# Performance work log

Measured on AMD Instinct MI355X. Metric: run time of the kernel, lower is better.

The kernel has to match this reference:

```python
import jax, jax.numpy as jnp
import numpy as np

N = 50000      # n_nodes
E = 300000     # n_edges
R = 32         # n_relations
D = 256        # embedding_dim
H = 128        # bilstm_hidden_size (2H == D so gate dims line up, as the source requires)
I = 64         # input_dim (time-series feature dim)
B = 4096       # batch
S = 50         # seq_len
HOPS = 2       # context_hops


def setup_inputs() -> dict:
    key = jax.random.key(0)
    ks = jax.random.split(key, 20)
    sc = 0.02
    inp = {
        "ts": jax.random.normal(ks[0], (B, S, I), jnp.float32),
        "node_emb": jax.random.normal(ks[1], (N, D), jnp.float32) * sc,
        "rel_w": jax.random.normal(ks[2], (R, D), jnp.float32) * sc + 1.0,
        "gate_W": jax.random.normal(ks[3], (D, 2 * D), jnp.float32) * sc,
        "gate_b": jnp.zeros((D,), jnp.float32),
        "risk_W1": jax.random.normal(ks[4], (D, D), jnp.float32) * sc,
        "risk_b1": jnp.zeros((D,), jnp.float32),
        "risk_W2": jax.random.normal(ks[5], (D, D), jnp.float32) * sc,
        "risk_b2": jnp.zeros((D,), jnp.float32),
        # BiLSTM encoder params (torch gate order i,f,g,o), fwd + bwd directions
        "Wih_f": jax.random.normal(ks[6], (4 * H, I), jnp.float32) * sc,
        "Whh_f": jax.random.normal(ks[7], (4 * H, H), jnp.float32) * sc,
        "b_f": jnp.zeros((4 * H,), jnp.float32),
        "Wih_b": jax.random.normal(ks[8], (4 * H, I), jnp.float32) * sc,
        "Whh_b": jax.random.normal(ks[9], (4 * H, H), jnp.float32) * sc,
        "b_b": jnp.zeros((4 * H,), jnp.float32),
        "edge_index": jax.random.randint(ks[10], (2, E), 0, N, jnp.int32),
        "edge_type": jax.random.randint(ks[11], (E,), 0, R, jnp.int32),
        "node_indexes": jax.random.randint(ks[12], (B,), 0, N, jnp.int32),
    }
    return inp


def _lstm_dir(x, Wih, Whh, b, reverse):
    # x: [B, S, I] -> outputs [B, S, H]
    def step(carry, xt):
        h, c = carry
        g = xt @ Wih.T + h @ Whh.T + b          # [B, 4H]
        i, f, gg, o = jnp.split(g, 4, axis=-1)
        c = jax.nn.sigmoid(f) * c + jax.nn.sigmoid(i) * jnp.tanh(gg)
        h = jax.nn.sigmoid(o) * jnp.tanh(c)
        return (h, c), h
    h0 = jnp.zeros((x.shape[0], Whh.shape[1]), x.dtype)
    xs = jnp.swapaxes(x, 0, 1)                   # [S, B, I]
    _, hs = jax.lax.scan(step, (h0, h0), xs, reverse=reverse)
    return jnp.swapaxes(hs, 0, 1)                # [B, S, H]


def _gcn(emb, head, tail, edge_type, rel_w, n_hops):
    # relation-weighted multi-hop message passing: gather -> relation scale -> scatter-mean
    deg = jax.ops.segment_sum(jnp.ones((head.shape[0],), emb.dtype), head, num_segments=N)
    deg = jnp.clip(deg, 1.0)[:, None]
    out = emb
    acc = emb
    for _ in range(n_hops):
        msg = out[tail] * rel_w[edge_type]                      # [E, D]
        out = jax.ops.segment_sum(msg, head, num_segments=N) / deg
        acc = acc + out
    return acc / (n_hops + 1.0)


def reference(ts, node_emb, rel_w, gate_W, gate_b, risk_W1, risk_b1, risk_W2,
              risk_b2, Wih_f, Whh_f, b_f, Wih_b, Whh_b, b_b,
              edge_index, edge_type, node_indexes):
    head, tail = edge_index[0], edge_index[1]
    all_emb = _gcn(node_emb, head, tail, edge_type, rel_w, HOPS)
    struct = all_emb[node_indexes]                              # [B, D]
    # BiLSTM encoder, temporal embedding = mean over time of [B,S,2H]
    hf = _lstm_dir(ts, Wih_f, Whh_f, b_f, reverse=False)
    hb = _lstm_dir(ts, Wih_b, Whh_b, b_b, reverse=True)
    temporal = jnp.concatenate([hf, hb], axis=-1).mean(axis=1)  # [B, 2H] == [B, D]
    cat = jnp.concatenate([struct, temporal], axis=-1)          # [B, 2D]
    gate = jax.nn.sigmoid(cat @ gate_W.T + gate_b)              # [B, D]
    merged = gate * struct + (1.0 - gate) * temporal
    risk = jnp.tanh(merged @ risk_W1.T + risk_b1) @ risk_W2.T + risk_b2
    return jax.nn.sigmoid(risk.sum(axis=-1))                    # [B]
```

## Files before the change

### kernel.cpp

```cpp
#include <hip/hip_runtime.h>

#define N_NODES 50000
#define N_EDGES 300000
#define DIM 256
#define HID 128
#define INP 64
#define BATCH 4096
#define SEQ 50
#define SCAN_BLOCKS 196

typedef float f32x2 __attribute__((ext_vector_type(2)));
typedef float f32x4 __attribute__((ext_vector_type(4)));
typedef __bf16 bf16x2 __attribute__((ext_vector_type(2)));
typedef __bf16 bf16x8 __attribute__((ext_vector_type(8)));

__device__ __forceinline__ float sigmoidf_(float x) {
    return __builtin_amdgcn_rcpf(1.0f + __expf(-x));
}
__device__ __forceinline__ float tanhf_(float x) {
    return 1.0f - 2.0f * __builtin_amdgcn_rcpf(1.0f + __expf(2.0f * x));
}


__global__ void k_hist(const int* __restrict__ head, int* __restrict__ deg) {
    int e = blockIdx.x * 256 + threadIdx.x;
    if (e < N_EDGES) atomicAdd(&deg[head[e]], 1);
}

__global__ void k_bsum(const int* __restrict__ deg, int* __restrict__ bsum) {
    __shared__ int red[256];
    int n = blockIdx.x * 256 + threadIdx.x;
    red[threadIdx.x] = (n < N_NODES) ? deg[n] : 0;
    __syncthreads();
    for (int st = 128; st > 0; st >>= 1) {
        if (threadIdx.x < st) red[threadIdx.x] += red[threadIdx.x + st];
        __syncthreads();
    }
    if (threadIdx.x == 0) bsum[blockIdx.x] = red[0];
}

__global__ void k_scanb(const int* __restrict__ bsum, int* __restrict__ boff) {
    __shared__ int s[256];
    int i = threadIdx.x;
    int v = (i < SCAN_BLOCKS) ? bsum[i] : 0;
    s[i] = v;
    __syncthreads();
    for (int st = 1; st < 256; st <<= 1) {
        int add = (i >= st) ? s[i - st] : 0;
        __syncthreads();
        s[i] += add;
        __syncthreads();
    }
    boff[i] = s[i] - v;
}

__global__ void k_scan2(const int* __restrict__ deg, const int* __restrict__ boff,
                        int* __restrict__ offsets, int* __restrict__ cursor) {
    __shared__ int s[256];
    int i = threadIdx.x;
    int n = blockIdx.x * 256 + i;
    int v = (n < N_NODES) ? deg[n] : 0;
    s[i] = v;
    __syncthreads();
    for (int st = 1; st < 256; st <<= 1) {
        int add = (i >= st) ? s[i - st] : 0;
        __syncthreads();
        s[i] += add;
        __syncthreads();
    }
    if (n < N_NODES) {
        int off = boff[blockIdx.x] + s[i] - v;
        offsets[n] = off;
        cursor[n] = off;
    }
    if (n == 0) offsets[N_NODES] = N_EDGES;
}

__global__ void k_place(const int* __restrict__ head, const int* __restrict__ tail,
                        const int* __restrict__ etype, int* __restrict__ cursor,
                        int* __restrict__ sorted) {
    int e = blockIdx.x * 256 + threadIdx.x;
    if (e >= N_EDGES) return;
    int h = head[e];
    int pos = atomicAdd(&cursor[h], 1);
    sorted[pos] = tail[e] | (etype[e] << 16);
}

__global__ void k_flag(const int* __restrict__ nidx, const int* __restrict__ offsets,
                       const int* __restrict__ sorted, char* __restrict__ flag) {
    int b = blockIdx.x * 256 + threadIdx.x;
    if (b >= BATCH) return;
    int n = nidx[b];
    flag[n] = 1;
    int s = offsets[n], e = offsets[n + 1];
    for (int j = s; j < e; j++) flag[sorted[j] & 0xFFFF] = 1;
}

__global__ void k_gather(const int* __restrict__ offsets, const int* __restrict__ sorted,
                         const float* __restrict__ relw, const float* __restrict__ src,
                         const char* __restrict__ flag, float* __restrict__ dst) {
    int tid = threadIdx.x;
    int w = tid >> 6, lane = tid & 63;
    int n = blockIdx.x * 4 + w;
    if (n >= N_NODES) return;
    if (!flag[n]) return;
    int s = offsets[n], e = offsets[n + 1];
    f32x4 acc0 = (f32x4){0.f, 0.f, 0.f, 0.f};
    f32x4 acc1 = (f32x4){0.f, 0.f, 0.f, 0.f};
    f32x4 acc2 = (f32x4){0.f, 0.f, 0.f, 0.f};
    f32x4 acc3 = (f32x4){0.f, 0.f, 0.f, 0.f};
    int j = s;
    for (; j + 4 <= e; j += 4) {
        int p0 = sorted[j], p1 = sorted[j + 1], p2 = sorted[j + 2], p3 = sorted[j + 3];
        f32x4 v0 = *(const f32x4*)(src + (size_t)(p0 & 0xFFFF) * DIM + lane * 4);
        f32x4 v1 = *(const f32x4*)(src + (size_t)(p1 & 0xFFFF) * DIM + lane * 4);
        f32x4 v2 = *(const f32x4*)(src + (size_t)(p2 & 0xFFFF) * DIM + lane * 4);
        f32x4 v3 = *(const f32x4*)(src + (size_t)(p3 & 0xFFFF) * DIM + lane * 4);
        acc0 += v0 * *(const f32x4*)(relw + (p0 >> 16) * DIM + lane * 4);
        acc1 += v1 * *(const f32x4*)(relw + (p1 >> 16) * DIM + lane * 4);
        acc2 += v2 * *(const f32x4*)(relw + (p2 >> 16) * DIM + lane * 4);
        acc3 += v3 * *(const f32x4*)(relw + (p3 >> 16) * DIM + lane * 4);
    }
    for (; j < e; j++) {
        int p0 = sorted[j];
        f32x4 v0 = *(const f32x4*)(src + (size_t)(p0 & 0xFFFF) * DIM + lane * 4);
        acc0 += v0 * *(const f32x4*)(relw + (p0 >> 16) * DIM + lane * 4);
    }
    acc0 = (acc0 + acc1) + (acc2 + acc3);
    float inv = 1.0f / fmaxf((float)(e - s), 1.0f);
    *(f32x4*)(dst + (size_t)n * DIM + lane * 4) = acc0 * inv;
}

__global__ void k_gather2(const int* __restrict__ nidx, const int* __restrict__ offsets,
                          const int* __restrict__ sorted, const float* __restrict__ relw,
                          const float* __restrict__ out1, const float* __restrict__ emb,
                          float* __restrict__ structb) {
    int tid = threadIdx.x;
    int w = tid >> 6, lane = tid & 63;
    int b = blockIdx.x * 4 + w;
    int n = nidx[b];
    int s = offsets[n], e = offsets[n + 1];
    f32x4 acc0 = (f32x4){0.f, 0.f, 0.f, 0.f};
    f32x4 acc1 = (f32x4){0.f, 0.f, 0.f, 0.f};
    f32x4 acc2 = (f32x4){0.f, 0.f, 0.f, 0.f};
    f32x4 acc3 = (f32x4){0.f, 0.f, 0.f, 0.f};
    int j = s;
    for (; j + 4 <= e; j += 4) {
        int p0 = sorted[j], p1 = sorted[j + 1], p2 = sorted[j + 2], p3 = sorted[j + 3];
        f32x4 v0 = *(const f32x4*)(out1 + (size_t)(p0 & 0xFFFF) * DIM + lane * 4);
        f32x4 v1 = *(const f32x4*)(out1 + (size_t)(p1 & 0xFFFF) * DIM + lane * 4);
        f32x4 v2 = *(const f32x4*)(out1 + (size_t)(p2 & 0xFFFF) * DIM + lane * 4);
        f32x4 v3 = *(const f32x4*)(out1 + (size_t)(p3 & 0xFFFF) * DIM + lane * 4);
        acc0 += v0 * *(const f32x4*)(relw + (p0 >> 16) * DIM + lane * 4);
        acc1 += v1 * *(const f32x4*)(relw + (p1 >> 16) * DIM + lane * 4);
        acc2 += v2 * *(const f32x4*)(relw + (p2 >> 16) * DIM + lane * 4);
        acc3 += v3 * *(const f32x4*)(relw + (p3 >> 16) * DIM + lane * 4);
    }
    for (; j < e; j++) {
        int p0 = sorted[j];
        f32x4 v0 = *(const f32x4*)(out1 + (size_t)(p0 & 0xFFFF) * DIM + lane * 4);
        acc0 += v0 * *(const f32x4*)(relw + (p0 >> 16) * DIM + lane * 4);
    }
    acc0 = (acc0 + acc1) + (acc2 + acc3);
    float inv = 1.0f / fmaxf((float)(e - s), 1.0f);
    f32x4 o2 = acc0 * inv;
    f32x4 e0 = *(const f32x4*)(emb + (size_t)n * DIM + lane * 4);
    f32x4 o1 = *(const f32x4*)(out1 + (size_t)n * DIM + lane * 4);
    *(f32x4*)(structb + (size_t)b * DIM + lane * 4) = (e0 + o1 + o2) * (1.0f / 3.0f);
}

__global__ void k_w2frag(const float* __restrict__ Wih_f, const float* __restrict__ Whh_f,
                         const float* __restrict__ Wih_b, const float* __restrict__ Whh_b,
                         __bf16* __restrict__ w2) {
    int idx = blockIdx.x * 256 + threadIdx.x;
    int dir = idx / 98304;
    int rem = idx % 98304;
    int frag = rem >> 9;
    int within = rem & 511;
    int lane = within >> 3, j = within & 7;
    int kc = frag % 6;
    int wg = frag / 6;
    int g = wg & 3, w = wg >> 2;
    int n = g * 128 + w * 16 + (lane & 15);
    int k = kc * 32 + (lane >> 4) * 8 + j;
    const float* Wih = dir ? Wih_b : Wih_f;
    const float* Whh = dir ? Whh_b : Whh_f;
    float v = (k < 64) ? Wih[n * 64 + k] : Whh[n * 128 + (k - 64)];
    w2[idx] = (__bf16)v;
}

__global__ void k_packw(const float* __restrict__ W, __bf16* __restrict__ dst,
                        int K, int total) {
    int idx = blockIdx.x * 256 + threadIdx.x;
    if (idx >= total) return;
    int frag = idx >> 9, within = idx & 511;
    int lane = within >> 3, j = within & 7;
    int kcN = K >> 5;
    int kc = frag % kcN, T = frag / kcN;
    int n = T * 16 + (lane & 15);
    int k = kc * 32 + (lane >> 4) * 8 + j;
    dst[idx] = (__bf16)W[(size_t)n * K + k];
}

__launch_bounds__(512)
__global__ void k_lstm(const float* __restrict__ ts, const __bf16* __restrict__ w2frag,
                       const float* __restrict__ b_f, const float* __restrict__ b_b,
                       float* __restrict__ temporal) {
    int dir = blockIdx.y;
    int btile = blockIdx.x;
    int tid = threadIdx.x;
    int w = tid >> 6;
    int lane = tid & 63;
    int col = lane & 15, quad = lane >> 4;

    __shared__ __align__(16) __bf16 A[16][200];

    for (int i = tid; i < 16 * 128; i += 512) {
        A[i >> 7][64 + (i & 127)] = (__bf16)0.0f;
    }

    const float* bias = dir ? b_b : b_f;
    float bv[4];
#pragma unroll
    for (int g = 0; g < 4; g++) {
        bv[g] = bias[g * 128 + w * 16 + col];
    }

    const __bf16* wbase = w2frag + (size_t)dir * 98304 + (size_t)w * 12288;
    bf16x8 wreg[24];
#pragma unroll
    for (int f = 0; f < 24; f++) {
        wreg[f] = *(const bf16x8*)(wbase + (f << 9) + lane * 8);
    }

    int sm = tid >> 5, sc = (tid & 31) * 2;
    const float* xbase = ts + ((size_t)(btile * 16 + sm) * SEQ) * INP + sc;
    f32x2 xpre = *(const f32x2*)(xbase + (size_t)(dir ? (SEQ - 1) : 0) * INP);

    f32x4 c_reg = (f32x4){0.f, 0.f, 0.f, 0.f};
    f32x4 hsum  = (f32x4){0.f, 0.f, 0.f, 0.f};
    int hoff = 64 + w * 16 + col;
    __syncthreads();

    for (int t = 0; t < SEQ; t++) {
        {
            bf16x2 xv;
            xv[0] = (__bf16)xpre.x; xv[1] = (__bf16)xpre.y;
            *(bf16x2*)&A[sm][sc] = xv;
        }
        if (t + 1 < SEQ) {
            int tt = dir ? (SEQ - 2 - t) : (t + 1);
            xpre = *(const f32x2*)(xbase + (size_t)tt * INP);
        }
        __syncthreads();

        f32x4 acc[4];
#pragma unroll
        for (int g = 0; g < 4; g++) {
            acc[g] = (f32x4){bv[g], bv[g], bv[g], bv[g]};
        }
#pragma unroll
        for (int kc = 0; kc < 6; kc++) {
            bf16x8 a0 = *(const bf16x8*)&A[col][kc * 32 + quad * 8];
#pragma unroll
            for (int g = 0; g < 4; g++) {
                acc[g] = __builtin_amdgcn_mfma_f32_16x16x32_bf16(a0, wreg[g * 6 + kc], acc[g], 0, 0, 0);
            }
        }
        __syncthreads();

#pragma unroll
        for (int r = 0; r < 4; r++) {
            float iv = acc[0][r];
            float fv = acc[1][r];
            float gv = acc[2][r];
            float ov = acc[3][r];
            float c = sigmoidf_(fv) * c_reg[r] + sigmoidf_(iv) * tanhf_(gv);
            float h = sigmoidf_(ov) * tanhf_(c);
            c_reg[r] = c;
            hsum[r] += h;
            A[quad * 4 + r][hoff] = (__bf16)h;
        }
    }

#pragma unroll
    for (int r = 0; r < 4; r++) {
        int b = btile * 16 + quad * 4 + r;
        int j = w * 16 + col;
        temporal[(size_t)b * 256 + dir * 128 + j] = hsum[r] * (1.0f / SEQ);
    }
}


__global__ void k_w2sum(const float* __restrict__ W2, const float* __restrict__ b2,
                        float* __restrict__ w2s) {
    int k = threadIdx.x;
    int bb = blockIdx.x;
    float s = 0.0f;
#pragma unroll
    for (int n = 0; n < 32; n++) s += W2[(size_t)(bb * 32 + n) * 256 + k];
    atomicAdd(&w2s[k], s);
    if (bb == 0) {
        __shared__ float red[256];
        red[k] = b2[k];
        __syncthreads();
        for (int st = 128; st > 0; st >>= 1) {
            if (k < st) red[k] += red[k + st];
            __syncthreads();
        }
        if (k == 0) atomicAdd(&w2s[256], red[0]);
    }
}

__launch_bounds__(256)
__global__ void k_head(const float* __restrict__ structb, const float* __restrict__ temporal,
                       const __bf16* __restrict__ gwp, const __bf16* __restrict__ w1p,
                       const float* __restrict__ gate_b, const float* __restrict__ risk_b1,
                       const float* __restrict__ w2s, float* __restrict__ out) {
    int bt = blockIdx.x;
    int tid = threadIdx.x;
    int w = tid >> 6, lane = tid & 63;
    int col = lane & 15, quad = lane >> 4;

    __shared__ __align__(16) __bf16 cat[16][520];
    __shared__ __align__(16) __bf16 mbuf[16][264];
    __shared__ float sacc[16];

    for (int i = tid; i < 16 * 512; i += 256) {
        int m = i >> 9, k = i & 511;
        int b = bt * 16 + m;
        float v = (k < 256) ? structb[(size_t)b * 256 + k]
                            : temporal[(size_t)b * 256 + (k - 256)];
        cat[m][k] = (__bf16)v;
    }
    if (tid < 16) sacc[tid] = 0.0f;
    __syncthreads();

    f32x4 acc[4];
#pragma unroll
    for (int ct = 0; ct < 4; ct++) {
        float b = gate_b[w * 64 + ct * 16 + col];
        acc[ct] = (f32x4){b, b, b, b};
    }
#pragma unroll
    for (int kc = 0; kc < 16; kc++) {
        bf16x8 a = *(const bf16x8*)&cat[col][kc * 32 + quad * 8];
#pragma unroll
        for (int ct = 0; ct < 4; ct++) {
            bf16x8 bf = *(const bf16x8*)(gwp + (((w * 4 + ct) * 16 + kc) << 9) + lane * 8);
            acc[ct] = __builtin_amdgcn_mfma_f32_16x16x32_bf16(a, bf, acc[ct], 0, 0, 0);
        }
    }
#pragma unroll
    for (int ct = 0; ct < 4; ct++) {
        int n = w * 64 + ct * 16 + col;
#pragma unroll
        for (int r = 0; r < 4; r++) {
            int m = quad * 4 + r;
            int b = bt * 16 + m;
            float g = sigmoidf_(acc[ct][r]);
            float s = structb[(size_t)b * 256 + n];
            float tm = temporal[(size_t)b * 256 + n];
            mbuf[m][n] = (__bf16)(g * s + (1.0f - g) * tm);
        }
    }
    __syncthreads();

    f32x4 acc2[4];
#pragma unroll
    for (int ct = 0; ct < 4; ct++) {
        float b = risk_b1[w * 64 + ct * 16 + col];
        acc2[ct] = (f32x4){b, b, b, b};
    }
#pragma unroll
    for (int kc = 0; kc < 8; kc++) {
        bf16x8 a = *(const bf16x8*)&mbuf[col][kc * 32 + quad * 8];
#pragma unroll
        for (int ct = 0; ct < 4; ct++) {
            bf16x8 bf = *(const bf16x8*)(w1p + (((w * 4 + ct) * 8 + kc) << 9) + lane * 8);
            acc2[ct] = __builtin_amdgcn_mfma_f32_16x16x32_bf16(a, bf, acc2[ct], 0, 0, 0);
        }
    }
    float part[4] = {0.f, 0.f, 0.f, 0.f};
#pragma unroll
    for (int ct = 0; ct < 4; ct++) {
        int n = w * 64 + ct * 16 + col;
        float wv = w2s[n];
#pragma unroll
        for (int r = 0; r < 4; r++) {
            part[r] += tanhf_(acc2[ct][r]) * wv;
        }
    }
#pragma unroll
    for (int off = 1; off < 16; off <<= 1) {
#pragma unroll
        for (int r = 0; r < 4; r++) part[r] += __shfl_xor(part[r], off, 64);
    }
    if (col == 0) {
#pragma unroll
        for (int r = 0; r < 4; r++) atomicAdd(&sacc[quad * 4 + r], part[r]);
    }
    __syncthreads();
    if (tid < 16) out[bt * 16 + tid] = sigmoidf_(sacc[tid] + w2s[256]);
}


extern "C" void kernel_launch(void* const* d_in, const int* in_sizes, int n_in,
                              void* d_out, int out_size, void* d_ws, size_t ws_size,
                              hipStream_t stream) {
    const float* ts       = (const float*)d_in[0];
    const float* node_emb = (const float*)d_in[1];
    const float* rel_w    = (const float*)d_in[2];
    const float* gate_W   = (const float*)d_in[3];
    const float* gate_b   = (const float*)d_in[4];
    const float* risk_W1  = (const float*)d_in[5];
    const float* risk_b1  = (const float*)d_in[6];
    const float* risk_W2  = (const float*)d_in[7];
    const float* risk_b2  = (const float*)d_in[8];
    const float* Wih_f    = (const float*)d_in[9];
    const float* Whh_f    = (const float*)d_in[10];
    const float* b_f      = (const float*)d_in[11];
    const float* Wih_b    = (const float*)d_in[12];
    const float* Whh_b    = (const float*)d_in[13];
    const float* b_b      = (const float*)d_in[14];
    const int* edge_index = (const int*)d_in[15];
    const int* edge_type  = (const int*)d_in[16];
    const int* node_idx   = (const int*)d_in[17];
    const int* head = edge_index;
    const int* tail = edge_index + N_EDGES;
    float* out = (float*)d_out;

    char* ws = (char*)d_ws;
    const size_t o_deg      = 0;
    const size_t o_flagbuf  = 200704;
    const size_t o_bsum     = o_flagbuf + 50176;
    const size_t o_boff     = o_bsum + 1024;
    const size_t o_offsets  = o_boff + 1024;
    const size_t o_cursor   = o_offsets + 200960;
    const size_t o_sorted   = o_cursor + 200704;
    const size_t o_out1     = o_sorted + 1200128;
    const size_t o_temporal = o_out1 + 51200000;
    const size_t o_struct   = o_temporal + 4194304;
    const size_t o_gwp      = o_struct + 4194304;
    const size_t o_w1p      = o_gwp + 262144;
    const size_t o_w2s      = o_w1p + 131072;
    const size_t o_w2frag   = o_w2s + 2048;

    int*    deg      = (int*)(ws + o_deg);
    char*   flag     = (char*)(ws + o_flagbuf);
    int*    bsum     = (int*)(ws + o_bsum);
    int*    boff     = (int*)(ws + o_boff);
    int*    offsets  = (int*)(ws + o_offsets);
    int*    cursor   = (int*)(ws + o_cursor);
    int*    sorted   = (int*)(ws + o_sorted);
    float*  out1     = (float*)(ws + o_out1);
    float*  temporal = (float*)(ws + o_temporal);
    float*  structb  = (float*)(ws + o_struct);
    __bf16* gwp      = (__bf16*)(ws + o_gwp);
    __bf16* w1p      = (__bf16*)(ws + o_w1p);
    float*  w2s      = (float*)(ws + o_w2s);
    __bf16* w2frag   = (__bf16*)(ws + o_w2frag);

    hipMemsetAsync(ws, 0, o_flagbuf + 50176, stream);
    hipMemsetAsync(w2s, 0, 2048, stream);

    k_w2frag<<<768, 256, 0, stream>>>(Wih_f, Whh_f, Wih_b, Whh_b, w2frag);
    k_packw<<<512, 256, 0, stream>>>(gate_W, gwp, 512, 256 * 512);
    k_packw<<<256, 256, 0, stream>>>(risk_W1, w1p, 256, 256 * 256);
    k_w2sum<<<8, 256, 0, stream>>>(risk_W2, risk_b2, w2s);
    k_hist<<<(N_EDGES + 255) / 256, 256, 0, stream>>>(head, deg);
    k_bsum<<<SCAN_BLOCKS, 256, 0, stream>>>(deg, bsum);
    k_scanb<<<1, 256, 0, stream>>>(bsum, boff);
    k_scan2<<<SCAN_BLOCKS, 256, 0, stream>>>(deg, boff, offsets, cursor);
    k_place<<<(N_EDGES + 255) / 256, 256, 0, stream>>>(head, tail, edge_type, cursor, sorted);
    k_flag<<<BATCH / 256, 256, 0, stream>>>(node_idx, offsets, sorted, flag);
    k_gather<<<(N_NODES + 3) / 4, 256, 0, stream>>>(offsets, sorted, rel_w, node_emb, flag, out1);
    k_lstm<<<dim3(BATCH / 16, 2), 512, 0, stream>>>(ts, w2frag, b_f, b_b, temporal);
    k_gather2<<<BATCH / 4, 256, 0, stream>>>(node_idx, offsets, sorted, rel_w, out1, node_emb, structb);
    k_head<<<BATCH / 16, 256, 0, stream>>>(structb, temporal, gwp, w1p, gate_b, risk_b1, w2s, out);
}
```

Baseline: 353.9 us.

## Interleave two batch tiles per LSTM block and fuse prep kernels into one launch

The LSTM kernel now handles two independent 16-row batch tiles per block and interleaves them. Each tile's MFMA matmul overlaps with the other tile's gate nonlinearities, using double-buffered shared memory, so the serial recurrence latency is hidden. This halves the grid to 128x2 blocks, which may underfill the GPU's compute units. Separately, the weight packing, W2 row-sum and buffer zeroing are merged into a single prep kernel, replacing two memsets and four launches.

```diff
diff --git a/kernel.cpp b/kernel.cpp
--- a/kernel.cpp
+++ b/kernel.cpp
@@ -19,6 +19,68 @@
 }
 __device__ __forceinline__ float tanhf_(float x) {
     return 1.0f - 2.0f * __builtin_amdgcn_rcpf(1.0f + __expf(2.0f * x));
+}
+
+__global__ void k_prep(const float* __restrict__ Wih_f, const float* __restrict__ Whh_f,
+                       const float* __restrict__ Wih_b, const float* __restrict__ Whh_b,
+                       const float* __restrict__ gate_W, const float* __restrict__ risk_W1,
+                       const float* __restrict__ risk_W2, const float* __restrict__ risk_b2,
+                       __bf16* __restrict__ w2frag, __bf16* __restrict__ gwp,
+                       __bf16* __restrict__ w1p, float* __restrict__ w2s,
+                       int* __restrict__ deg, int* __restrict__ flagi) {
+    __shared__ float red[256];
+    int bid = blockIdx.x, tid = threadIdx.x;
+    if (bid < 768) {
+        int idx = bid * 256 + tid;
+        int dir = idx / 98304;
+        int rem = idx % 98304;
+        int frag = rem >> 9;
+        int within = rem & 511;
+        int lane = within >> 3, j = within & 7;
+        int kc = frag % 6;
+        int wg = frag / 6;
+        int g = wg & 3, w = wg >> 2;
+        int n = g * 128 + w * 16 + (lane & 15);
+        int k = kc * 32 + (lane >> 4) * 8 + j;
+        const float* Wih = dir ? Wih_b : Wih_f;
+        const float* Whh = dir ? Whh_b : Whh_f;
+        float v = (k < 64) ? Wih[n * 64 + k] : Whh[n * 128 + (k - 64)];
+        w2frag[idx] = (__bf16)v;
+    } else if (bid < 1280) {
+        int idx = (bid - 768) * 256 + tid;
+        int frag = idx >> 9, within = idx & 511;
+        int lane = within >> 3, j = within & 7;
+        int kc = frag % 16, T = frag / 16;
+        int n = T * 16 + (lane & 15);
+        int k = kc * 32 + (lane >> 4) * 8 + j;
+        gwp[idx] = (__bf16)gate_W[(size_t)n * 512 + k];
+    } else if (bid < 1536) {
+        int idx = (bid - 1280) * 256 + tid;
+        int frag = idx >> 9, within = idx & 511;
+        int lane = within >> 3, j = within & 7;
+        int kc = frag % 8, T = frag / 8;
+        int n = T * 16 + (lane & 15);
+        int k = kc * 32 + (lane >> 4) * 8 + j;
+        w1p[idx] = (__bf16)risk_W1[(size_t)n * 256 + k];
+    } else if (bid == 1536) {
+        int k = tid;
+        float s = 0.0f;
+        for (int n = 0; n < 256; n++) s += risk_W2[(size_t)n * 256 + k];
+        w2s[k] = s;
+        red[k] = risk_b2[k];
+        __syncthreads();
+        for (int st = 128; st > 0; st >>= 1) {
+            if (k < st) red[k] += red[k + st];
+            __syncthreads();
+        }
+        if (k == 0) w2s[256] = red[0];
+    } else if (bid < 1733) {
+        int i = (bid - 1537) * 256 + tid;
+        if (i < N_NODES) deg[i] = 0;
+    } else {
+        int i = (bid - 1733) * 256 + tid;
+        flagi[i] = 0;
+    }
 }
 
 
@@ -169,39 +231,6 @@
     *(f32x4*)(structb + (size_t)b * DIM + lane * 4) = (e0 + o1 + o2) * (1.0f / 3.0f);
 }
 
-__global__ void k_w2frag(const float* __restrict__ Wih_f, const float* __restrict__ Whh_f,
-                         const float* __restrict__ Wih_b, const float* __restrict__ Whh_b,
-                         __bf16* __restrict__ w2) {
-    int idx = blockIdx.x * 256 + threadIdx.x;
-    int dir = idx / 98304;
-    int rem = idx % 98304;
-    int frag = rem >> 9;
-    int within = rem & 511;
-    int lane = within >> 3, j = within & 7;
-    int kc = frag % 6;
-    int wg = frag / 6;
-    int g = wg & 3, w = wg >> 2;
-    int n = g * 128 + w * 16 + (lane & 15);
-    int k = kc * 32 + (lane >> 4) * 8 + j;
-    const float* Wih = dir ? Wih_b : Wih_f;
-    const float* Whh = dir ? Whh_b : Whh_f;
-    float v = (k < 64) ? Wih[n * 64 + k] : Whh[n * 128 + (k - 64)];
-    w2[idx] = (__bf16)v;
-}
-
-__global__ void k_packw(const float* __restrict__ W, __bf16* __restrict__ dst,
-                        int K, int total) {
-    int idx = blockIdx.x * 256 + threadIdx.x;
-    if (idx >= total) return;
-    int frag = idx >> 9, within = idx & 511;
-    int lane = within >> 3, j = within & 7;
-    int kcN = K >> 5;
-    int kc = frag % kcN, T = frag / kcN;
-    int n = T * 16 + (lane & 15);
-    int k = kc * 32 + (lane >> 4) * 8 + j;
-    dst[idx] = (__bf16)W[(size_t)n * K + k];
-}
-
 __launch_bounds__(512)
 __global__ void k_lstm(const float* __restrict__ ts, const __bf16* __restrict__ w2frag,
                        const float* __restrict__ b_f, const float* __restrict__ b_b,
@@ -213,18 +242,19 @@
     int lane = tid & 63;
     int col = lane & 15, quad = lane >> 4;
 
-    __shared__ __align__(16) __bf16 A[16][200];
-
-    for (int i = tid; i < 16 * 128; i += 512) {
-        A[i >> 7][64 + (i & 127)] = (__bf16)0.0f;
+    __shared__ __align__(16) __bf16 SA[2 * 16 * 200];
+    __shared__ __align__(16) __bf16 SB[2 * 16 * 200];
+
+    for (int i = tid; i < 2048; i += 512) {
+        int m = i >> 7, k = i & 127;
+        SA[m * 200 + 64 + k] = (__bf16)0.0f;
+        SB[m * 200 + 64 + k] = (__bf16)0.0f;
     }
 
     const float* bias = dir ? b_b : b_f;
     float bv[4];
 #pragma unroll
-    for (int g = 0; g < 4; g++) {
-        bv[g] = bias[g * 128 + w * 16 + col];
-    }
+    for (int g = 0; g < 4; g++) bv[g] = bias[g * 128 + w * 16 + col];
 
     const __bf16* wbase = w2frag + (size_t)dir * 98304 + (size_t)w * 12288;
     bf16x8 wreg[24];
@@ -234,83 +264,109 @@
     }
 
     int sm = tid >> 5, sc = (tid & 31) * 2;
-    const float* xbase = ts + ((size_t)(btile * 16 + sm) * SEQ) * INP + sc;
-    f32x2 xpre = *(const f32x2*)(xbase + (size_t)(dir ? (SEQ - 1) : 0) * INP);
-
-    f32x4 c_reg = (f32x4){0.f, 0.f, 0.f, 0.f};
-    f32x4 hsum  = (f32x4){0.f, 0.f, 0.f, 0.f};
-    int hoff = 64 + w * 16 + col;
-    __syncthreads();
+    const float* xbA = ts + ((size_t)(btile * 32 + sm) * SEQ) * INP + sc;
+    const float* xbB = ts + ((size_t)(btile * 32 + 16 + sm) * SEQ) * INP + sc;
+    int t0i = dir ? (SEQ - 1) : 0;
+    int t1i = dir ? (SEQ - 2) : 1;
+    {
+        f32x2 xa = *(const f32x2*)(xbA + (size_t)t0i * INP);
+        f32x2 xb = *(const f32x2*)(xbB + (size_t)t0i * INP);
+        bf16x2 va; va[0] = (__bf16)xa.x; va[1] = (__bf16)xa.y;
+        bf16x2 vb; vb[0] = (__bf16)xb.x; vb[1] = (__bf16)xb.y;
+        *(bf16x2*)&SA[sm * 200 + sc] = va;
+        *(bf16x2*)&SB[sm * 200 + sc] = vb;
+    }
+    f32x2 xpreA = *(const f32x2*)(xbA + (size_t)t1i * INP);
+    f32x2 xpreB = *(const f32x2*)(xbB + (size_t)t1i * INP);
+
+    f32x4 cA = (f32x4){0.f, 0.f, 0.f, 0.f}, hsA = cA;
+    f32x4 cB = cA, hsB = cA;
+    f32x4 accA[4], accB[4];
+    int hwr = quad * 4 * 200 + 64 + w * 16 + col;
+    int ard = col * 200 + quad * 8;
+    __syncthreads();
+
+#pragma unroll
+    for (int g = 0; g < 4; g++) accA[g] = (f32x4){bv[g], bv[g], bv[g], bv[g]};
+#pragma unroll
+    for (int kc = 0; kc < 6; kc++) {
+        bf16x8 a0 = *(const bf16x8*)&SA[ard + kc * 32];
+#pragma unroll
+        for (int g = 0; g < 4; g++)
+            accA[g] = __builtin_amdgcn_mfma_f32_16x16x32_bf16(a0, wreg[g * 6 + kc], accA[g], 0, 0, 0);
+    }
 
     for (int t = 0; t < SEQ; t++) {
-        {
-            bf16x2 xv;
-            xv[0] = (__bf16)xpre.x; xv[1] = (__bf16)xpre.y;
-            *(bf16x2*)&A[sm][sc] = xv;
+        int cb = (t & 1) * 3200;
+        int nb = ((t + 1) & 1) * 3200;
+
+#pragma unroll
+        for (int g = 0; g < 4; g++) accB[g] = (f32x4){bv[g], bv[g], bv[g], bv[g]};
+#pragma unroll
+        for (int kc = 0; kc < 6; kc++) {
+            bf16x8 a0 = *(const bf16x8*)&SB[cb + ard + kc * 32];
+#pragma unroll
+            for (int g = 0; g < 4; g++)
+                accB[g] = __builtin_amdgcn_mfma_f32_16x16x32_bf16(a0, wreg[g * 6 + kc], accB[g], 0, 0, 0);
+        }
+#pragma unroll
+        for (int r = 0; r < 4; r++) {
+            float c = sigmoidf_(accA[1][r]) * cA[r] + sigmoidf_(accA[0][r]) * tanhf_(accA[2][r]);
+            float h = sigmoidf_(accA[3][r]) * tanhf_(c);
+            cA[r] = c;
+            hsA[r] += h;
+            SA[nb + hwr + r * 200] = (__bf16)h;
         }
         if (t + 1 < SEQ) {
-            int tt = dir ? (SEQ - 2 - t) : (t + 1);
-            xpre = *(const f32x2*)(xbase + (size_t)tt * INP);
-        }
-        __syncthreads();
-
-        f32x4 acc[4];
-#pragma unroll
-        for (int g = 0; g < 4; g++) {
-            acc[g] = (f32x4){bv[g], bv[g], bv[g], bv[g]};
-        }
-#pragma unroll
-        for (int kc = 0; kc < 6; kc++) {
-            bf16x8 a0 = *(const bf16x8*)&A[col][kc * 32 + quad * 8];
-#pragma unroll
-            for (int g = 0; g < 4; g++) {
-                acc[g] = __builtin_amdgcn_mfma_f32_16x16x32_bf16(a0, wreg[g * 6 + kc], acc[g], 0, 0, 0);
+            bf16x2 v; v[0] = (__bf16)xpreA.x; v[1] = (__bf16)xpreA.y;
+            *(bf16x2*)&SA[nb + sm * 200 + sc] = v;
+            if (t + 2 < SEQ) {
+                int ti = dir ? (SEQ - 3 - t) : (t + 2);
+                xpreA = *(const f32x2*)(xbA + (size_t)ti * INP);
             }
         }
         __syncthreads();
 
+        if (t + 1 < SEQ) {
+#pragma unroll
+            for (int g = 0; g < 4; g++) accA[g] = (f32x4){bv[g], bv[g], bv[g], bv[g]};
+#pragma unroll
+            for (int kc = 0; kc < 6; kc++) {
+                bf16x8 a0 = *(const bf16x8*)&SA[nb + ard + kc * 32];
+#pragma unroll
+                for (int g = 0; g < 4; g++)
+                    accA[g] = __builtin_amdgcn_mfma_f32_16x16x32_bf16(a0, wreg[g * 6 + kc], accA[g], 0, 0, 0);
+            }
+        }
 #pragma unroll
         for (int r = 0; r < 4; r++) {
-            float iv = acc[0][r];
-            float fv = acc[1][r];
-            float gv = acc[2][r];
-            float ov = acc[3][r];
-            float c = sigmoidf_(fv) * c_reg[r] + sigmoidf_(iv) * tanhf_(gv);
-            float h = sigmoidf_(ov) * tanhf_(c);
-            c_reg[r] = c;
-            hsum[r] += h;
-            A[quad * 4 + r][hoff] = (__bf16)h;
-        }
+            float c = sigmoidf_(accB[1][r]) * cB[r] + sigmoidf_(accB[0][r]) * tanhf_(accB[2][r]);
+            float h = sigmoidf_(accB[3][r]) * tanhf_(c);
+            cB[r] = c;
+            hsB[r] += h;
+            SB[nb + hwr + r * 200] = (__bf16)h;
+        }
+        if (t + 1 < SEQ) {
+            bf16x2 v; v[0] = (__bf16)xpreB.x; v[1] = (__bf16)xpreB.y;
+            *(bf16x2*)&SB[nb + sm * 200 + sc] = v;
+            if (t + 2 < SEQ) {
+                int ti = dir ? (SEQ - 3 - t) : (t + 2);
+                xpreB = *(const f32x2*)(xbB + (size_t)ti * INP);
+            }
+        }
+        __syncthreads();
     }
 
 #pragma unroll
     for (int r = 0; r < 4; r++) {
-        int b = btile * 16 + quad * 4 + r;
         int j = w * 16 + col;
-        temporal[(size_t)b * 256 + dir * 128 + j] = hsum[r] * (1.0f / SEQ);
-    }
-}
-
-
-__global__ void k_w2sum(const float* __restrict__ W2, const float* __restrict__ b2,
-                        float* __restrict__ w2s) {
-    int k = threadIdx.x;
-    int bb = blockIdx.x;
-    float s = 0.0f;
-#pragma unroll
-    for (int n = 0; n < 32; n++) s += W2[(size_t)(bb * 32 + n) * 256 + k];
-    atomicAdd(&w2s[k], s);
-    if (bb == 0) {
-        __shared__ float red[256];
-        red[k] = b2[k];
-        __syncthreads();
-        for (int st = 128; st > 0; st >>= 1) {
-            if (k < st) red[k] += red[k + st];
-            __syncthreads();
-        }
-        if (k == 0) atomicAdd(&w2s[256], red[0]);
-    }
-}
+        int bA = btile * 32 + quad * 4 + r;
+        int bB = bA + 16;
+        temporal[(size_t)bA * 256 + dir * 128 + j] = hsA[r] * (1.0f / SEQ);
+        temporal[(size_t)bB * 256 + dir * 128 + j] = hsB[r] * (1.0f / SEQ);
+    }
+}
+
 
 __launch_bounds__(256)
 __global__ void k_head(const float* __restrict__ structb, const float* __restrict__ temporal,
@@ -448,6 +504,7 @@
 
     int*    deg      = (int*)(ws + o_deg);
     char*   flag     = (char*)(ws + o_flagbuf);
+    int*    flagi    = (int*)(ws + o_flagbuf);
     int*    bsum     = (int*)(ws + o_bsum);
     int*    boff     = (int*)(ws + o_boff);
     int*    offsets  = (int*)(ws + o_offsets);
@@ -461,13 +518,8 @@
     float*  w2s      = (float*)(ws + o_w2s);
     __bf16* w2frag   = (__bf16*)(ws + o_w2frag);
 
-    hipMemsetAsync(ws, 0, o_flagbuf + 50176, stream);
-    hipMemsetAsync(w2s, 0, 2048, stream);
-
-    k_w2frag<<<768, 256, 0, stream>>>(Wih_f, Whh_f, Wih_b, Whh_b, w2frag);
-    k_packw<<<512, 256, 0, stream>>>(gate_W, gwp, 512, 256 * 512);
-    k_packw<<<256, 256, 0, stream>>>(risk_W1, w1p, 256, 256 * 256);
-    k_w2sum<<<8, 256, 0, stream>>>(risk_W2, risk_b2, w2s);
+    k_prep<<<1782, 256, 0, stream>>>(Wih_f, Whh_f, Wih_b, Whh_b, gate_W, risk_W1,
+                                     risk_W2, risk_b2, w2frag, gwp, w1p, w2s, deg, flagi);
     k_hist<<<(N_EDGES + 255) / 256, 256, 0, stream>>>(head, deg);
     k_bsum<<<SCAN_BLOCKS, 256, 0, stream>>>(deg, bsum);
     k_scanb<<<1, 256, 0, stream>>>(bsum, boff);
@@ -475,7 +527,7 @@
     k_place<<<(N_EDGES + 255) / 256, 256, 0, stream>>>(head, tail, edge_type, cursor, sorted);
     k_flag<<<BATCH / 256, 256, 0, stream>>>(node_idx, offsets, sorted, flag);
     k_gather<<<(N_NODES + 3) / 4, 256, 0, stream>>>(offsets, sorted, rel_w, node_emb, flag, out1);
-    k_lstm<<<dim3(BATCH / 16, 2), 512, 0, stream>>>(ts, w2frag, b_f, b_b, temporal);
+    k_lstm<<<dim3(BATCH / 32, 2), 512, 0, stream>>>(ts, w2frag, b_f, b_b, temporal);
     k_gather2<<<BATCH / 4, 256, 0, stream>>>(node_idx, offsets, sorted, rel_w, out1, node_emb, structb);
     k_head<<<BATCH / 16, 256, 0, stream>>>(structb, temporal, gwp, w1p, gate_b, risk_b1, w2s, out);
 }
```

Measured after the change: 338.4 us. 1.05x faster.
